# Kernel optimization log

Measured on AMD Instinct MI355X. Metric: run time of the kernel, lower is better.

Reference implementation:

```python
import jax, jax.numpy as jnp
import numpy as np

D_MODEL = 1024
NUM_HEADS = 16
HEAD_DIM = D_MODEL // NUM_HEADS
THETA = 10000.0


def setup_inputs() -> dict:
    key = jax.random.key(0)
    k1, k2, k3 = jax.random.split(key, 3)
    B, S = 4, 2048
    std_qkv = (2.0 / (D_MODEL + 3 * D_MODEL)) ** 0.5
    std_out = (2.0 / (D_MODEL + D_MODEL)) ** 0.5
    return {
        "x": jax.random.normal(k1, (B, S, D_MODEL), dtype=jnp.float32),
        "token_positions": jnp.arange(S, dtype=jnp.int64 if jax.config.jax_enable_x64 else jnp.int32),
        "w_qkv": jax.random.normal(k2, (3 * D_MODEL, D_MODEL), dtype=jnp.float32) * std_qkv,
        "w_out": jax.random.normal(k3, (D_MODEL, D_MODEL), dtype=jnp.float32) * std_out,
    }


def _apply_rope(x, token_positions):
    # x: [b, h, s, d_h]; token_positions: [s]
    inv_freq = 1.0 / (THETA ** (jnp.arange(0, HEAD_DIM, 2, dtype=jnp.float32) / HEAD_DIM))
    angles = token_positions.astype(jnp.float32)[:, None] * inv_freq  # [s, d_h/2]
    cos, sin = jnp.cos(angles), jnp.sin(angles)
    x_even = x[..., 0::2]
    x_odd = x[..., 1::2]
    out_even = x_even * cos - x_odd * sin
    out_odd = x_even * sin + x_odd * cos
    # re-interleave even/odd lanes
    return jnp.stack([out_even, out_odd], axis=-1).reshape(x.shape)


def reference(x, token_positions, w_qkv, w_out):
    B, S, _ = x.shape
    qkv = jnp.einsum("bsd,ed->bse", x, w_qkv)  # [b, s, 3*d_model]
    q, k, v = jnp.split(qkv, 3, axis=-1)

    def to_heads(t):  # [b, s, d_model] -> [b, h, s, d_h]
        return t.reshape(B, S, NUM_HEADS, HEAD_DIM).transpose(0, 2, 1, 3)

    q, k, v = to_heads(q), to_heads(k), to_heads(v)
    q = _apply_rope(q, token_positions)
    k = _apply_rope(k, token_positions)

    scale = 1.0 / (HEAD_DIM ** 0.5)
    scores = jnp.einsum("bhqd,bhkd->bhqk", q, k) * scale  # [b, h, s, s]
    causal = jnp.tril(jnp.ones((S, S), dtype=bool))
    scores = jnp.where(causal, scores, -jnp.inf)
    probs = jax.nn.softmax(scores, axis=-1)
    out = jnp.einsum("bhqk,bhkd->bhqd", probs, v)  # [b, h, s, d_h]
    out = out.transpose(0, 2, 1, 3).reshape(B, S, D_MODEL)
    return jnp.einsum("bsd,ed->bse", out, w_out)
```

## Files before the change

kernel.cpp:

```cpp
#include <hip/hip_runtime.h>

typedef unsigned short u16;
typedef __attribute__((ext_vector_type(4))) float f32x4;
typedef __attribute__((ext_vector_type(8))) __bf16 bf16x8;
typedef __attribute__((ext_vector_type(4))) __bf16 bf16x4;
typedef __attribute__((ext_vector_type(8))) short short8;
typedef __attribute__((ext_vector_type(4))) u16 u16x4;

__device__ __forceinline__ u16 f2bf(float f) {
    union { float f; unsigned u; } v; v.f = f;
    unsigned r = v.u + 0x7fffu + ((v.u >> 16) & 1u);
    return (u16)(r >> 16);
}

__device__ __forceinline__ f32x4 mfma16(bf16x8 a, bf16x8 b, f32x4 c) {
    return __builtin_amdgcn_mfma_f32_16x16x32_bf16(a, b, c, 0, 0, 0);
}

__device__ __forceinline__ void gload16(const u16* g, u16* lds) {
    __builtin_amdgcn_global_load_lds(
        (const __attribute__((address_space(1))) void*)g,
        (__attribute__((address_space(3))) void*)lds, 16, 0, 0);
}

__global__ void cvt_bf16_kernel(const float* __restrict__ src, u16* __restrict__ dst, int n4) {
    int i = blockIdx.x * blockDim.x + threadIdx.x;
    if (i >= n4) return;
    float4 v = ((const float4*)src)[i];
    u16x4 o = { f2bf(v.x), f2bf(v.y), f2bf(v.z), f2bf(v.w) };
    *(u16x4*)&dst[i * 4] = o;
}

__global__ void rope_tbl_kernel(const int* __restrict__ pos, float2* __restrict__ tbl) {
    int i = blockIdx.x * blockDim.x + threadIdx.x;
    int s = i >> 5, p = i & 31;
    float inv = powf(10000.0f, -(float)p / 32.0f);
    float a = (float)pos[s] * inv;
    float sn, cs;
    sincosf(a, &sn, &cs);
    tbl[i] = make_float2(cs, sn);
}

template<int MODE>
__global__ __launch_bounds__(256) void gemm_bt(
    const u16* __restrict__ A, const u16* __restrict__ B,
    float* __restrict__ C, int N,
    u16* __restrict__ Qt, u16* __restrict__ Ktn, u16* __restrict__ VTt,
    const float2* __restrict__ tbl)
{
    __shared__ alignas(16) u16 As[128 * 32];
    __shared__ alignas(16) u16 Bs[128 * 32];
    const int t = threadIdx.x;
    const int l = t & 63, w = t >> 6;
    const int lg = l >> 4, lc = l & 15;
    const int wr = w >> 1, wc = w & 1;
    const int brow = blockIdx.y * 128, bcol = blockIdx.x * 128;
    const int sr = w * 16 + (l >> 2), sc = (l & 3) * 8;
    const u16* ga = A + (size_t)(brow + sr) * 1024 + sc;
    const u16* gb = B + (size_t)(bcol + sr) * 1024 + sc;
    u16* la = &As[w * 512];
    u16* lb = &Bs[w * 512];
    f32x4 acc[4][4] = {};

    for (int kt = 0; kt < 1024; kt += 32) {
        __syncthreads();
        gload16(ga + kt, la);
        gload16(ga + 64 * 1024 + kt, la + 2048);
        gload16(gb + kt, lb);
        gload16(gb + 64 * 1024 + kt, lb + 2048);
        __syncthreads();
        bf16x8 af[4], bfr[4];
#pragma unroll
        for (int i = 0; i < 4; ++i)
            af[i] = *(const bf16x8*)&As[(wr * 64 + i * 16 + lc) * 32 + lg * 8];
#pragma unroll
        for (int j = 0; j < 4; ++j)
            bfr[j] = *(const bf16x8*)&Bs[(wc * 64 + j * 16 + lc) * 32 + lg * 8];
#pragma unroll
        for (int i = 0; i < 4; ++i)
#pragma unroll
            for (int j = 0; j < 4; ++j)
                acc[i][j] = mfma16(af[i], bfr[j], acc[i][j]);
    }

    if (MODE == 0) {
#pragma unroll
        for (int i = 0; i < 4; ++i) {
            int row = brow + wr * 64 + i * 16 + lg * 4;
#pragma unroll
            for (int j = 0; j < 4; ++j) {
                int col = bcol + wc * 64 + j * 16 + lc;
#pragma unroll
                for (int jj = 0; jj < 4; ++jj)
                    C[(size_t)(row + jj) * N + col] = acc[i][j][jj];
            }
        }
    } else {
        const int b = brow >> 11;
#pragma unroll
        for (int i = 0; i < 4; ++i) {
            int s0 = (brow & 2047) + wr * 64 + i * 16 + lg * 4;
#pragma unroll
            for (int j = 0; j < 4; ++j) {
                int e0 = bcol + wc * 64 + j * 16;
                int region = e0 >> 10;
                int er = e0 & 1023;
                int h = er >> 6;
                int d = (er & 63) + lc;
                size_t bh = (size_t)(b * 16 + h);
                if (region <= 1) {
                    int p = d >> 1;
                    float sgn = (d & 1) ? 1.0f : -1.0f;
                    u16* dst = (region == 0) ? Qt : Ktn;
                    float mul = (region == 0) ? 0.18033688011112043f : 1.0f;
#pragma unroll
                    for (int jj = 0; jj < 4; ++jj) {
                        float v = acc[i][j][jj];
                        float pr = __shfl_xor(v, 1);
                        float2 cs = tbl[(size_t)(s0 + jj) * 32 + p];
                        float o = (v * cs.x + pr * cs.y * sgn) * mul;
                        dst[(bh * 2048 + s0 + jj) * 64 + d] = f2bf(o);
                    }
                } else {
                    u16x4 pk;
#pragma unroll
                    for (int jj = 0; jj < 4; ++jj) pk[jj] = f2bf(acc[i][j][jj]);
                    *(u16x4*)&VTt[(bh * 64 + d) * 2048 + s0] = pk;
                }
            }
        }
    }
}

__global__ __launch_bounds__(256) void attn_kernel(
    const u16* __restrict__ Qt, const u16* __restrict__ Kt,
    const u16* __restrict__ VTt, u16* __restrict__ O)
{
    __shared__ alignas(16) u16 Kl[64 * 72];
    __shared__ alignas(16) u16 Vl[64 * 72];
    const int bid = blockIdx.x;
    const int qt = 15 - (bid >> 6);
    const int bh = bid & 63;
    const int t = threadIdx.x, l = t & 63, w = t >> 6;
    const int lg = l >> 4, lc = l & 15;
    const int qb0 = qt * 128 + w * 32;

    bf16x8 qf[2][2];
#pragma unroll
    for (int f = 0; f < 2; ++f)
#pragma unroll
        for (int fk = 0; fk < 2; ++fk)
            qf[f][fk] = *(const bf16x8*)&Qt[((size_t)bh * 2048 + qb0 + 16 * f + lc) * 64 + fk * 32 + lg * 8];

    f32x4 aco[2][4] = {};
    float m[2] = { -1e30f, -1e30f }, ls[2] = { 0.f, 0.f };
    const int ntiles = 2 * qt + 2;

    const int r = t >> 2, cg = t & 3;
    const u16* gkp = Kt + (size_t)bh * 131072 + r * 64 + cg * 16;
    const u16* gvp = VTt + (size_t)bh * 131072 + (size_t)r * 2048 + cg * 16;
    u16* wk = &Kl[r * 72 + cg * 16];
    u16* wv = &Vl[r * 72 + cg * 16];

    short8 rk0 = *(const short8*)(gkp);
    short8 rk1 = *(const short8*)(gkp + 8);
    short8 rv0 = *(const short8*)(gvp);
    short8 rv1 = *(const short8*)(gvp + 8);

    for (int kt = 0; kt < ntiles; ++kt) {
        const int kv0 = kt * 64;
        __syncthreads();
        *(short8*)wk = rk0; *(short8*)(wk + 8) = rk1;
        *(short8*)wv = rv0; *(short8*)(wv + 8) = rv1;
        if (kt + 1 < ntiles) {
            const int nx = kv0 + 64;
            rk0 = *(const short8*)(gkp + (size_t)nx * 64);
            rk1 = *(const short8*)(gkp + (size_t)nx * 64 + 8);
            rv0 = *(const short8*)(gvp + nx);
            rv1 = *(const short8*)(gvp + nx + 8);
        }
        __syncthreads();

        const int act0 = (kv0 <= qb0 + 15);
        const int act1 = (kv0 <= qb0 + 31);

        f32x4 sc[2][4];
        const f32x4 zf = { 0.f, 0.f, 0.f, 0.f };
#pragma unroll
        for (int nb = 0; nb < 4; ++nb) {
            bf16x8 kb0 = *(const bf16x8*)&Kl[(nb * 16 + lc) * 72 + lg * 8];
            bf16x8 kb1 = *(const bf16x8*)&Kl[(nb * 16 + lc) * 72 + 32 + lg * 8];
            if (act0) {
                sc[0][nb] = mfma16(kb0, qf[0][0], zf);
                sc[0][nb] = mfma16(kb1, qf[0][1], sc[0][nb]);
            }
            if (act1) {
                sc[1][nb] = mfma16(kb0, qf[1][0], zf);
                sc[1][nb] = mfma16(kb1, qf[1][1], sc[1][nb]);
            }
        }

        float pm[2] = { -1e38f, -1e38f };
#pragma unroll
        for (int f = 0; f < 2; ++f) {
            const int act = f ? act1 : act0;
            if (!act) continue;
            const int qq = qb0 + 16 * f + lc;
            if (kv0 + 63 > qb0 + 16 * f) {
#pragma unroll
                for (int nb = 0; nb < 4; ++nb)
#pragma unroll
                    for (int jj = 0; jj < 4; ++jj) {
                        int kk = kv0 + nb * 16 + lg * 4 + jj;
                        if (kk > qq) sc[f][nb][jj] = -1e38f;
                    }
            }
            float a0 = fmaxf(fmaxf(sc[f][0][0], sc[f][0][1]), fmaxf(sc[f][0][2], sc[f][0][3]));
            float a1 = fmaxf(fmaxf(sc[f][1][0], sc[f][1][1]), fmaxf(sc[f][1][2], sc[f][1][3]));
            float a2 = fmaxf(fmaxf(sc[f][2][0], sc[f][2][1]), fmaxf(sc[f][2][2], sc[f][2][3]));
            float a3 = fmaxf(fmaxf(sc[f][3][0], sc[f][3][1]), fmaxf(sc[f][3][2], sc[f][3][3]));
            float a = fmaxf(fmaxf(a0, a1), fmaxf(a2, a3));
            a = fmaxf(a, __shfl_xor(a, 16));
            a = fmaxf(a, __shfl_xor(a, 32));
            pm[f] = a;
        }

        int need = ((act0 && pm[0] > m[0] + 11.0f) || (act1 && pm[1] > m[1] + 11.0f));
        if (__any(need)) {
#pragma unroll
            for (int f = 0; f < 2; ++f) {
                float mn = fmaxf(m[f], pm[f]);
                float scal = exp2f(m[f] - mn);
                m[f] = mn;
                ls[f] *= scal;
#pragma unroll
                for (int nb = 0; nb < 4; ++nb) aco[f][nb] *= scal;
            }
        }

        bf16x8 pB[2][2];
#pragma unroll
        for (int f = 0; f < 2; ++f) {
            const int act = f ? act1 : act0;
            if (!act) continue;
            float lsf = 0.f;
#pragma unroll
            for (int nb = 0; nb < 4; ++nb)
#pragma unroll
                for (int jj = 0; jj < 4; ++jj) {
                    float p = exp2f(sc[f][nb][jj] - m[f]);
                    sc[f][nb][jj] = p;
                    lsf += p;
                }
            ls[f] += lsf;
#pragma unroll
            for (int fk = 0; fk < 2; ++fk) {
                bf16x8 pb;
#pragma unroll
                for (int e = 0; e < 4; ++e) {
                    pb[e]     = (__bf16)sc[f][2 * fk][e];
                    pb[e + 4] = (__bf16)sc[f][2 * fk + 1][e];
                }
                pB[f][fk] = pb;
            }
        }

#pragma unroll
        for (int nb = 0; nb < 4; ++nb) {
#pragma unroll
            for (int fk = 0; fk < 2; ++fk) {
                bf16x4 vlo = *(const bf16x4*)&Vl[(nb * 16 + lc) * 72 + fk * 32 + lg * 4];
                bf16x4 vhi = *(const bf16x4*)&Vl[(nb * 16 + lc) * 72 + fk * 32 + 16 + lg * 4];
                bf16x8 va = __builtin_shufflevector(vlo, vhi, 0, 1, 2, 3, 4, 5, 6, 7);
                if (act0) aco[0][nb] = mfma16(va, pB[0][fk], aco[0][nb]);
                if (act1) aco[1][nb] = mfma16(va, pB[1][fk], aco[1][nb]);
            }
        }
    }

    const int b = bh >> 4, h = bh & 15;
#pragma unroll
    for (int f = 0; f < 2; ++f) {
        float s = ls[f];
        s += __shfl_xor(s, 16);
        s += __shfl_xor(s, 32);
        float rinv = 1.0f / s;
        size_t row = (size_t)b * 2048 + qb0 + 16 * f + lc;
#pragma unroll
        for (int nb = 0; nb < 4; ++nb) {
            u16x4 pk;
#pragma unroll
            for (int jj = 0; jj < 4; ++jj) pk[jj] = f2bf(aco[f][nb][jj] * rinv);
            *(u16x4*)&O[row * 1024 + h * 64 + nb * 16 + lg * 4] = pk;
        }
    }
}

extern "C" void kernel_launch(void* const* d_in, const int* in_sizes, int n_in,
                              void* d_out, int out_size, void* d_ws, size_t ws_size,
                              hipStream_t stream) {
    const float* x    = (const float*)d_in[0];
    const int*   pos  = (const int*)d_in[1];
    const float* wqkv = (const float*)d_in[2];
    const float* wout = (const float*)d_in[3];
    float* out = (float*)d_out;
    char* ws = (char*)d_ws;

    u16*    x_bf    = (u16*)(ws);
    u16*    wqkv_bf = (u16*)(ws + 16777216);
    u16*    wout_bf = (u16*)(ws + 23068672);
    float2* tbl     = (float2*)(ws + 25165824);
    u16*    Qt      = (u16*)(ws + 25690112);
    u16*    Kt      = (u16*)(ws + 42467328);
    u16*    VTt     = (u16*)(ws + 59244544);
    u16*    O       = (u16*)(ws + 76021760);
    if (ws_size < 92798976u) return;

    cvt_bf16_kernel<<<8192, 256, 0, stream>>>(x, x_bf, 2097152);
    cvt_bf16_kernel<<<3072, 256, 0, stream>>>(wqkv, wqkv_bf, 786432);
    cvt_bf16_kernel<<<1024, 256, 0, stream>>>(wout, wout_bf, 262144);
    rope_tbl_kernel<<<256, 256, 0, stream>>>(pos, tbl);

    dim3 g1(24, 64);
    gemm_bt<1><<<g1, 256, 0, stream>>>(x_bf, wqkv_bf, nullptr, 0, Qt, Kt, VTt, tbl);

    attn_kernel<<<1024, 256, 0, stream>>>(Qt, Kt, VTt, O);

    dim3 g2(8, 64);
    gemm_bt<0><<<g2, 256, 0, stream>>>(O, wout_bf, out, 1024, nullptr, nullptr, nullptr, nullptr);
}
```

Baseline: 309.4 us.

## Swizzle K/V layouts, use direct-to-LDS loads and smaller attention blocks

The QKV GEMM epilogue now writes K with an XOR swizzle and V^T in a permuted, swizzled tile order, so the attention kernel can fill unpadded LDS tiles with global_load_lds. It can then read K and V as full bf16x8 vectors without bank conflicts. The attention kernel moves to 128-thread blocks covering 64 query rows, which doubles the grid and drops the per-wave active checks. The softmax row sum is now computed with an MFMA against a ones vector instead of scalar adds and shuffles. The trade-off is that the register prefetch double-buffering is gone, so loads are no longer overlapped with compute, and the block now issues extra MFMAs for the row sums.

```diff
diff --git a/kernel.cpp b/kernel.cpp
--- a/kernel.cpp
+++ b/kernel.cpp
@@ -3,7 +3,6 @@
 typedef unsigned short u16;
 typedef __attribute__((ext_vector_type(4))) float f32x4;
 typedef __attribute__((ext_vector_type(8))) __bf16 bf16x8;
-typedef __attribute__((ext_vector_type(4))) __bf16 bf16x4;
 typedef __attribute__((ext_vector_type(8))) short short8;
 typedef __attribute__((ext_vector_type(4))) u16 u16x4;
 
@@ -119,31 +118,38 @@
                         float pr = __shfl_xor(v, 1);
                         float2 cs = tbl[(size_t)(s0 + jj) * 32 + p];
                         float o = (v * cs.x + pr * cs.y * sgn) * mul;
-                        dst[(bh * 2048 + s0 + jj) * 64 + d] = f2bf(o);
+                        int s = s0 + jj;
+                        int dd = (region == 0) ? d : (d ^ ((s & 7) << 3));
+                        dst[((size_t)bh * 2048 + s) * 64 + dd] = f2bf(o);
                     }
                 } else {
+                    int tile = s0 >> 6, r = s0 & 63;
+                    int p0 = ((r >> 5) << 5) + (((r >> 2) & 3) << 3) + (((r >> 4) & 1) << 2);
+                    int idx = (tile << 6) + (p0 ^ ((d & 7) << 3));
                     u16x4 pk;
 #pragma unroll
                     for (int jj = 0; jj < 4; ++jj) pk[jj] = f2bf(acc[i][j][jj]);
-                    *(u16x4*)&VTt[(bh * 64 + d) * 2048 + s0] = pk;
+                    *(u16x4*)&VTt[((size_t)bh * 64 + d) * 2048 + idx] = pk;
                 }
             }
         }
     }
 }
 
-__global__ __launch_bounds__(256) void attn_kernel(
-    const u16* __restrict__ Qt, const u16* __restrict__ Kt,
-    const u16* __restrict__ VTt, u16* __restrict__ O)
+__global__ __launch_bounds__(128, 4) void attn_kernel(
+    const u16* __restrict__ Qt, const u16* __restrict__ Kswz,
+    const u16* __restrict__ Vp, u16* __restrict__ O)
 {
-    __shared__ alignas(16) u16 Kl[64 * 72];
-    __shared__ alignas(16) u16 Vl[64 * 72];
+    __shared__ alignas(16) u16 Kl[64 * 64];
+    __shared__ alignas(16) u16 Vl[64 * 64];
     const int bid = blockIdx.x;
-    const int qt = 15 - (bid >> 6);
+    const int qt = 31 - (bid >> 6);
     const int bh = bid & 63;
     const int t = threadIdx.x, l = t & 63, w = t >> 6;
     const int lg = l >> 4, lc = l & 15;
-    const int qb0 = qt * 128 + w * 32;
+    const int qb0 = qt * 64 + w * 32;
+    const int ntiles = qt + 1;
+    const int swz = (lc & 7) << 3;
 
     bf16x8 qf[2][2];
 #pragma unroll
@@ -152,68 +158,54 @@
         for (int fk = 0; fk < 2; ++fk)
             qf[f][fk] = *(const bf16x8*)&Qt[((size_t)bh * 2048 + qb0 + 16 * f + lc) * 64 + fk * 32 + lg * 8];
 
+    const bf16x8 ones = { (__bf16)1.f, (__bf16)1.f, (__bf16)1.f, (__bf16)1.f,
+                          (__bf16)1.f, (__bf16)1.f, (__bf16)1.f, (__bf16)1.f };
+
     f32x4 aco[2][4] = {};
-    float m[2] = { -1e30f, -1e30f }, ls[2] = { 0.f, 0.f };
-    const int ntiles = 2 * qt + 2;
-
-    const int r = t >> 2, cg = t & 3;
-    const u16* gkp = Kt + (size_t)bh * 131072 + r * 64 + cg * 16;
-    const u16* gvp = VTt + (size_t)bh * 131072 + (size_t)r * 2048 + cg * 16;
-    u16* wk = &Kl[r * 72 + cg * 16];
-    u16* wv = &Vl[r * 72 + cg * 16];
-
-    short8 rk0 = *(const short8*)(gkp);
-    short8 rk1 = *(const short8*)(gkp + 8);
-    short8 rv0 = *(const short8*)(gvp);
-    short8 rv1 = *(const short8*)(gvp + 8);
+    f32x4 aco_sum[2] = {};
+    float m[2] = { -1e30f, -1e30f };
+
+    const int sr = l >> 3;
+    const int scq = (l & 7) * 8;
+    const u16* gK = Kswz + (size_t)bh * 131072 + scq;
+    const u16* gV = Vp + (size_t)bh * 131072 + scq;
 
     for (int kt = 0; kt < ntiles; ++kt) {
         const int kv0 = kt * 64;
         __syncthreads();
-        *(short8*)wk = rk0; *(short8*)(wk + 8) = rk1;
-        *(short8*)wv = rv0; *(short8*)(wv + 8) = rv1;
-        if (kt + 1 < ntiles) {
-            const int nx = kv0 + 64;
-            rk0 = *(const short8*)(gkp + (size_t)nx * 64);
-            rk1 = *(const short8*)(gkp + (size_t)nx * 64 + 8);
-            rv0 = *(const short8*)(gvp + nx);
-            rv1 = *(const short8*)(gvp + nx + 8);
+#pragma unroll
+        for (int j = 0; j < 4; ++j) {
+            const int rb = w * 32 + j * 8;
+            gload16(gK + (((size_t)(kv0 + rb + sr)) << 6), &Kl[rb * 64]);
+            gload16(gV + (size_t)(rb + sr) * 2048 + kv0, &Vl[rb * 64]);
         }
         __syncthreads();
-
-        const int act0 = (kv0 <= qb0 + 15);
-        const int act1 = (kv0 <= qb0 + 31);
 
         f32x4 sc[2][4];
         const f32x4 zf = { 0.f, 0.f, 0.f, 0.f };
 #pragma unroll
         for (int nb = 0; nb < 4; ++nb) {
-            bf16x8 kb0 = *(const bf16x8*)&Kl[(nb * 16 + lc) * 72 + lg * 8];
-            bf16x8 kb1 = *(const bf16x8*)&Kl[(nb * 16 + lc) * 72 + 32 + lg * 8];
-            if (act0) {
-                sc[0][nb] = mfma16(kb0, qf[0][0], zf);
-                sc[0][nb] = mfma16(kb1, qf[0][1], sc[0][nb]);
-            }
-            if (act1) {
-                sc[1][nb] = mfma16(kb0, qf[1][0], zf);
-                sc[1][nb] = mfma16(kb1, qf[1][1], sc[1][nb]);
-            }
-        }
-
-        float pm[2] = { -1e38f, -1e38f };
+            const u16* kr = &Kl[(nb * 16 + lc) * 64];
+            bf16x8 kb0 = *(const bf16x8*)&kr[(lg * 8) ^ swz];
+            bf16x8 kb1 = *(const bf16x8*)&kr[(32 + lg * 8) ^ swz];
+            sc[0][nb] = mfma16(kb0, qf[0][0], zf);
+            sc[0][nb] = mfma16(kb1, qf[0][1], sc[0][nb]);
+            sc[1][nb] = mfma16(kb0, qf[1][0], zf);
+            sc[1][nb] = mfma16(kb1, qf[1][1], sc[1][nb]);
+        }
+
+        float pm[2];
 #pragma unroll
         for (int f = 0; f < 2; ++f) {
-            const int act = f ? act1 : act0;
-            if (!act) continue;
-            const int qq = qb0 + 16 * f + lc;
             if (kv0 + 63 > qb0 + 16 * f) {
-#pragma unroll
-                for (int nb = 0; nb < 4; ++nb)
-#pragma unroll
-                    for (int jj = 0; jj < 4; ++jj) {
-                        int kk = kv0 + nb * 16 + lg * 4 + jj;
-                        if (kk > qq) sc[f][nb][jj] = -1e38f;
-                    }
+                const int qq = qb0 + 16 * f + lc;
+#pragma unroll
+                for (int nb = 0; nb < 4; ++nb) {
+                    const int kb = kv0 + nb * 16 + lg * 4;
+#pragma unroll
+                    for (int jj = 0; jj < 4; ++jj)
+                        if (kb + jj > qq) sc[f][nb][jj] = -1e38f;
+                }
             }
             float a0 = fmaxf(fmaxf(sc[f][0][0], sc[f][0][1]), fmaxf(sc[f][0][2], sc[f][0][3]));
             float a1 = fmaxf(fmaxf(sc[f][1][0], sc[f][1][1]), fmaxf(sc[f][1][2], sc[f][1][3]));
@@ -225,14 +217,14 @@
             pm[f] = a;
         }
 
-        int need = ((act0 && pm[0] > m[0] + 11.0f) || (act1 && pm[1] > m[1] + 11.0f));
+        int need = (pm[0] > m[0] + 11.0f) || (pm[1] > m[1] + 11.0f);
         if (__any(need)) {
 #pragma unroll
             for (int f = 0; f < 2; ++f) {
                 float mn = fmaxf(m[f], pm[f]);
                 float scal = exp2f(m[f] - mn);
                 m[f] = mn;
-                ls[f] *= scal;
+                aco_sum[f][0] *= scal;
 #pragma unroll
                 for (int nb = 0; nb < 4; ++nb) aco[f][nb] *= scal;
             }
@@ -241,18 +233,11 @@
         bf16x8 pB[2][2];
 #pragma unroll
         for (int f = 0; f < 2; ++f) {
-            const int act = f ? act1 : act0;
-            if (!act) continue;
-            float lsf = 0.f;
 #pragma unroll
             for (int nb = 0; nb < 4; ++nb)
 #pragma unroll
-                for (int jj = 0; jj < 4; ++jj) {
-                    float p = exp2f(sc[f][nb][jj] - m[f]);
-                    sc[f][nb][jj] = p;
-                    lsf += p;
-                }
-            ls[f] += lsf;
+                for (int jj = 0; jj < 4; ++jj)
+                    sc[f][nb][jj] = exp2f(sc[f][nb][jj] - m[f]);
 #pragma unroll
             for (int fk = 0; fk < 2; ++fk) {
                 bf16x8 pb;
@@ -267,24 +252,25 @@
 
 #pragma unroll
         for (int nb = 0; nb < 4; ++nb) {
+            const u16* vr = &Vl[(nb * 16 + lc) * 64];
 #pragma unroll
             for (int fk = 0; fk < 2; ++fk) {
-                bf16x4 vlo = *(const bf16x4*)&Vl[(nb * 16 + lc) * 72 + fk * 32 + lg * 4];
-                bf16x4 vhi = *(const bf16x4*)&Vl[(nb * 16 + lc) * 72 + fk * 32 + 16 + lg * 4];
-                bf16x8 va = __builtin_shufflevector(vlo, vhi, 0, 1, 2, 3, 4, 5, 6, 7);
-                if (act0) aco[0][nb] = mfma16(va, pB[0][fk], aco[0][nb]);
-                if (act1) aco[1][nb] = mfma16(va, pB[1][fk], aco[1][nb]);
-            }
+                bf16x8 va = *(const bf16x8*)&vr[(fk * 32 + lg * 8) ^ swz];
+                aco[0][nb] = mfma16(va, pB[0][fk], aco[0][nb]);
+                aco[1][nb] = mfma16(va, pB[1][fk], aco[1][nb]);
+            }
+        }
+#pragma unroll
+        for (int f = 0; f < 2; ++f) {
+            aco_sum[f] = mfma16(ones, pB[f][0], aco_sum[f]);
+            aco_sum[f] = mfma16(ones, pB[f][1], aco_sum[f]);
         }
     }
 
     const int b = bh >> 4, h = bh & 15;
 #pragma unroll
     for (int f = 0; f < 2; ++f) {
-        float s = ls[f];
-        s += __shfl_xor(s, 16);
-        s += __shfl_xor(s, 32);
-        float rinv = 1.0f / s;
+        float rinv = 1.0f / aco_sum[f][0];
         size_t row = (size_t)b * 2048 + qb0 + 16 * f + lc;
 #pragma unroll
         for (int nb = 0; nb < 4; ++nb) {
@@ -324,7 +310,7 @@
     dim3 g1(24, 64);
     gemm_bt<1><<<g1, 256, 0, stream>>>(x_bf, wqkv_bf, nullptr, 0, Qt, Kt, VTt, tbl);
 
-    attn_kernel<<<1024, 256, 0, stream>>>(Qt, Kt, VTt, O);
+    attn_kernel<<<2048, 128, 0, stream>>>(Qt, Kt, VTt, O);
 
     dim3 g2(8, 64);
     gemm_bt<0><<<g2, 256, 0, stream>>>(O, wout_bf, out, 1024, nullptr, nullptr, nullptr, nullptr);
```

Result: slower. 320.6 us (+3.6%).
